# Optimization experiments

Measured on AMD Instinct MI355X. Metric: run time of the kernel, lower is better.

## Reference

```python
import jax, jax.numpy as jnp
import numpy as np

L = 4096   # seq len (Lq == Lk, self-attention)
B = 8      # batch
D = 1024   # d_model
H = 16     # num heads
BUCKET = 32
FUTURE = 0


def setup_inputs() -> dict:
    key = jax.random.key(0)
    ks = jax.random.split(key, 9)
    q = jax.random.normal(ks[0], (L, B, D), jnp.float32)
    k = jax.random.normal(ks[1], (L, B, D), jnp.float32)
    v = jax.random.normal(ks[2], (L, B, D), jnp.float32)
    # one random element per bucket of size BUCKET (deterministic stand-in for
    # the module's no_grad sample_index); pin first sample to 0 so no query row
    # is fully masked under the causal mask.
    nb = L // BUCKET
    offs = jax.random.randint(ks[3], (nb,), 0, BUCKET)
    sampled_index = (jnp.arange(nb, dtype=jnp.int64) * BUCKET + offs).at[0].set(0)
    key_length = jax.random.randint(ks[4], (B,), L // 2, L + 1).astype(jnp.int64)
    # nn.MultiheadAttention params
    in_proj_weight = jax.random.normal(ks[5], (3 * D, D), jnp.float32) * 0.02
    in_proj_bias = jax.random.normal(ks[6], (3 * D,), jnp.float32) * 0.02
    out_w = jax.random.normal(ks[7], (D, D), jnp.float32) * 0.02
    out_b = jax.random.normal(ks[8], (D,), jnp.float32) * 0.02
    return {"q": q, "k": k, "v": v, "key_length": key_length,
            "sampled_index": sampled_index, "in_proj_weight": in_proj_weight,
            "in_proj_bias": in_proj_bias, "out_w": out_w, "out_b": out_b}


def reference(q, k, v, key_length, sampled_index, in_proj_weight, in_proj_bias, out_w, out_b):
    S = sampled_index.shape[0]
    dh = D // H
    # bucket-sampled gather of keys/values: [S, B, D]
    ks_ = k[sampled_index]
    vs_ = v[sampled_index]
    # modify_key_length: number of sampled indices inside each sequence's valid span
    mkl = jnp.sum((sampled_index[None, :] < key_length[:, None]).astype(jnp.int32), axis=1)  # [B]
    key_padding = jnp.arange(S)[None, :] >= mkl[:, None]                                      # [B, S] True = pad
    # causal mask on sampled indices: query i may attend to sample s iff i + future >= s
    causal = (jnp.arange(L)[:, None] + FUTURE) < sampled_index[None, :]                       # [Lq, S] True = masked
    mask = causal[None, None, :, :] | key_padding[:, None, None, :]                           # [B, 1, Lq, S]
    # in-projection (torch linear: x @ W.T + b)
    Wq, Wk, Wv = jnp.split(in_proj_weight, 3, axis=0)
    bq, bk, bv = jnp.split(in_proj_bias, 3)
    qp = (q @ Wq.T + bq).reshape(L, B, H, dh)
    kp = (ks_ @ Wk.T + bk).reshape(S, B, H, dh)
    vp = (vs_ @ Wv.T + bv).reshape(S, B, H, dh)
    scale = 1.0 / np.sqrt(dh).astype(np.float32)
    scores = jnp.einsum('qbhd,kbhd->bhqk', qp, kp) * scale
    scores = jnp.where(mask, -jnp.inf, scores)
    attn = jax.nn.softmax(scores, axis=-1)
    ctx = jnp.einsum('bhqk,kbhd->qbhd', attn, vp).reshape(L, B, D)
    return ctx @ out_w.T + out_b
```

## Files before the change

kernel.cpp:

```cpp
#include <hip/hip_runtime.h>
#include <hip/hip_bf16.h>

#define L_SEQ 4096
#define BATCH 8
#define DMODEL 1024
#define NHEAD 16
#define DHEAD 64
#define NSAMP 128

typedef __attribute__((ext_vector_type(8))) short short8;
typedef __attribute__((ext_vector_type(4))) float f32x4;

static __device__ __forceinline__ unsigned short f2bf(float f) {
    union { float f; unsigned int u; } x; x.f = f;
    unsigned int r = (x.u + 0x7fffu + ((x.u >> 16) & 1u)) >> 16;
    return (unsigned short)r;
}

static __device__ __forceinline__ void gld_lds16(const unsigned short* g,
                                                 unsigned short* l) {
    __builtin_amdgcn_global_load_lds(
        (const __attribute__((address_space(1))) void*)g,
        (__attribute__((address_space(3))) void*)l, 16, 0, 0);
}

__global__ void conv_bf16_kernel(const float* __restrict__ src,
                                 unsigned short* __restrict__ dst, int n4) {
    int idx = blockIdx.x * blockDim.x + threadIdx.x;
    if (idx < n4) {
        float4 v = ((const float4*)src)[idx];
        uint2 pk;
        pk.x = (unsigned)f2bf(v.x) | ((unsigned)f2bf(v.y) << 16);
        pk.y = (unsigned)f2bf(v.z) | ((unsigned)f2bf(v.w) << 16);
        ((uint2*)dst)[idx] = pk;
    }
}

__global__ void gather_bf16_kernel(const float* __restrict__ src,
                                   const int* __restrict__ smp,
                                   unsigned short* __restrict__ dst, int total8) {
    int idx = blockIdx.x * blockDim.x + threadIdx.x;
    if (idx < total8) {
        int s = idx >> 10;
        int rem = idx & 1023;
        const float* g = src + (size_t)smp[s] * (BATCH * DMODEL) + rem * 8;
        float4 v0 = *(const float4*)g;
        float4 v1 = *(const float4*)(g + 4);
        uint4 pk;
        pk.x = (unsigned)f2bf(v0.x) | ((unsigned)f2bf(v0.y) << 16);
        pk.y = (unsigned)f2bf(v0.z) | ((unsigned)f2bf(v0.w) << 16);
        pk.z = (unsigned)f2bf(v1.x) | ((unsigned)f2bf(v1.y) << 16);
        pk.w = (unsigned)f2bf(v1.z) | ((unsigned)f2bf(v1.w) << 16);
        *(uint4*)&dst[(size_t)idx * 8] = pk;
    }
}

__global__ void mkl_kernel(const int* __restrict__ smp,
                           const int* __restrict__ klen, int* __restrict__ mkl) {
    int b = threadIdx.x;
    if (b < BATCH) {
        int kl = klen[b];
        int c = 0;
        for (int s = 0; s < NSAMP; ++s) c += (smp[s] < kl) ? 1 : 0;
        mkl[b] = c;
    }
}

template <bool OUT_F32>
static __device__ __forceinline__ void gemm_body(
    const unsigned short* __restrict__ A, const unsigned short* __restrict__ Bw,
    const float* __restrict__ bias, void* __restrict__ Cp,
    int m0, int n0, int N, int K,
    unsigned short* lA, unsigned short* lB) {
    const int t = threadIdx.x;
    const int wave = t >> 6;
    const int lane = t & 63;
    const int l16 = lane & 15;
    const int quad = lane >> 4;
    const int wm = (wave >> 1) * 64;
    const int wn = (wave & 1) * 64;

    f32x4 acc[4][4];
    #pragma unroll
    for (int i = 0; i < 4; ++i)
        #pragma unroll
        for (int j = 0; j < 4; ++j)
            acc[i][j] = f32x4{0.f, 0.f, 0.f, 0.f};

    const int lin0 = t * 8;
    const int wbase = (t & ~63) * 8;

    for (int k0 = 0; k0 < K; k0 += 64) {
        #pragma unroll
        for (int p = 0; p < 4; ++p) {
            int lin = p * 2048 + lin0;
            int row = lin >> 6, col = lin & 63;
            gld_lds16(A + (size_t)(m0 + row) * K + k0 + col, lA + p * 2048 + wbase);
        }
        #pragma unroll
        for (int p = 0; p < 4; ++p) {
            int lin = p * 2048 + lin0;
            int row = lin >> 6, col = lin & 63;
            gld_lds16(Bw + (size_t)(n0 + row) * K + k0 + col, lB + p * 2048 + wbase);
        }
        __syncthreads();

        #pragma unroll
        for (int kk = 0; kk < 64; kk += 32) {
            short8 af[4], bfr[4];
            #pragma unroll
            for (int mt = 0; mt < 4; ++mt)
                af[mt] = *(const short8*)&lA[(wm + mt * 16 + l16) * 64 + kk + quad * 8];
            #pragma unroll
            for (int nt = 0; nt < 4; ++nt)
                bfr[nt] = *(const short8*)&lB[(wn + nt * 16 + l16) * 64 + kk + quad * 8];
            #pragma unroll
            for (int mt = 0; mt < 4; ++mt)
                #pragma unroll
                for (int nt = 0; nt < 4; ++nt)
                    acc[mt][nt] = __builtin_amdgcn_mfma_f32_16x16x32_bf16(
                        af[mt], bfr[nt], acc[mt][nt], 0, 0, 0);
        }
        __syncthreads();
    }

    #pragma unroll
    for (int mt = 0; mt < 4; ++mt) {
        #pragma unroll
        for (int nt = 0; nt < 4; ++nt) {
            int col = n0 + wn + nt * 16 + l16;
            float bv = bias[col];
            #pragma unroll
            for (int r = 0; r < 4; ++r) {
                int row = m0 + wm + mt * 16 + quad * 4 + r;
                float val = acc[mt][nt][r] + bv;
                if (OUT_F32)
                    ((float*)Cp)[(size_t)row * N + col] = val;
                else
                    ((unsigned short*)Cp)[(size_t)row * N + col] = f2bf(val);
            }
        }
    }
}

__global__ __launch_bounds__(256) void gemm_kv(
    const unsigned short* __restrict__ Ak, const unsigned short* __restrict__ Av,
    const unsigned short* __restrict__ Bk, const unsigned short* __restrict__ Bv,
    const float* __restrict__ bk, const float* __restrict__ bv,
    unsigned short* __restrict__ Ck, unsigned short* __restrict__ Cv) {
    __shared__ __align__(16) unsigned short lA[128 * 64];
    __shared__ __align__(16) unsigned short lB[128 * 64];
    if (blockIdx.z == 0)
        gemm_body<false>(Ak, Bk, bk, Ck, blockIdx.x * 128, blockIdx.y * 128,
                         DMODEL, DMODEL, lA, lB);
    else
        gemm_body<false>(Av, Bv, bv, Cv, blockIdx.x * 128, blockIdx.y * 128,
                         DMODEL, DMODEL, lA, lB);
}

#define GNT 32

template <bool OUT_F32>
__global__ __launch_bounds__(512, 2) void gemm256_kernel(
    const unsigned short* __restrict__ A, const unsigned short* __restrict__ Bw,
    const float* __restrict__ bias, void* __restrict__ Cp)
{
    __shared__ __align__(16) unsigned short ls[4][2][8192];

    const int bid = blockIdx.x;
    const int swz = (bid & 7) * 64 + (bid >> 3);
    const int m0 = (swz >> 2) * 256;
    const int n0 = (swz & 3) * 256;

    const int t = threadIdx.x;
    const int wave = t >> 6, lane = t & 63;
    const int l16 = lane & 15, quad = lane >> 4;
    const int wm = wave >> 2, wn = wave & 3;
    const int wb = wave * 512;

    const int srow = t >> 2;
    const int scol = (t & 3) * 8;
    const unsigned short* a0 = A + (size_t)(m0 + srow) * DMODEL + scol;
    const unsigned short* a1 = a0 + (size_t)128 * DMODEL;
    const unsigned short* b0 = Bw + (size_t)(n0 + srow) * DMODEL + scol;
    const unsigned short* b1 = b0 + (size_t)128 * DMODEL;

    #define STAGE(tk, s) do {                                   \
        gld_lds16(a0 + (tk) * 32, &ls[s][0][wb]);               \
        gld_lds16(a1 + (tk) * 32, &ls[s][0][4096 + wb]);        \
        gld_lds16(b0 + (tk) * 32, &ls[s][1][wb]);               \
        gld_lds16(b1 + (tk) * 32, &ls[s][1][4096 + wb]);        \
    } while (0)

    STAGE(0, 0); STAGE(1, 1); STAGE(2, 2);

    f32x4 acc[8][4];
    #pragma unroll
    for (int i = 0; i < 8; ++i)
        #pragma unroll
        for (int j = 0; j < 4; ++j)
            acc[i][j] = f32x4{0.f, 0.f, 0.f, 0.f};

    const int aoff = (wm * 128 + l16) * 32 + quad * 8;
    const int boff = (wn * 64 + l16) * 32 + quad * 8;

    #pragma unroll
    for (int tk = 0; tk < GNT; ++tk) {
        if (tk < GNT - 2)
            asm volatile("s_waitcnt vmcnt(8)" ::: "memory");
        else if (tk == GNT - 2)
            asm volatile("s_waitcnt vmcnt(4)" ::: "memory");
        else
            asm volatile("s_waitcnt vmcnt(0)" ::: "memory");
        __builtin_amdgcn_s_barrier();

        if (tk + 3 < GNT) STAGE(tk + 3, (tk + 3) & 3);

        const unsigned short* As = &ls[tk & 3][0][0];
        const unsigned short* Bs = &ls[tk & 3][1][0];
        short8 af[8], bq[4];
        #pragma unroll
        for (int nt = 0; nt < 4; ++nt)
            bq[nt] = *(const short8*)&Bs[boff + nt * 512];
        #pragma unroll
        for (int mt = 0; mt < 8; ++mt)
            af[mt] = *(const short8*)&As[aoff + mt * 512];

        __builtin_amdgcn_s_setprio(1);
        #pragma unroll
        for (int mt = 0; mt < 8; ++mt)
            #pragma unroll
            for (int nt = 0; nt < 4; ++nt)
                acc[mt][nt] = __builtin_amdgcn_mfma_f32_16x16x32_bf16(
                    af[mt], bq[nt], acc[mt][nt], 0, 0, 0);
        __builtin_amdgcn_s_setprio(0);
    }
    #undef STAGE

    #pragma unroll
    for (int mt = 0; mt < 8; ++mt) {
        #pragma unroll
        for (int nt = 0; nt < 4; ++nt) {
            int col = n0 + wn * 64 + nt * 16 + l16;
            float bv = bias[col];
            #pragma unroll
            for (int r = 0; r < 4; ++r) {
                int row = m0 + wm * 128 + mt * 16 + quad * 4 + r;
                float val = acc[mt][nt][r] + bv;
                if (OUT_F32)
                    ((float*)Cp)[(size_t)row * DMODEL + col] = val;
                else
                    ((unsigned short*)Cp)[(size_t)row * DMODEL + col] = f2bf(val);
            }
        }
    }
}

#define KST 72
#define VST 136
__global__ __launch_bounds__(256) void attn_kernel(
    const unsigned short* __restrict__ qp,
    const unsigned short* __restrict__ kp,
    const unsigned short* __restrict__ vp,
    const int* __restrict__ smp_g,
    const int* __restrict__ mkl_g,
    unsigned short* __restrict__ ctx)
{
    __shared__ __align__(16) unsigned short kbuf[NSAMP * KST];
    __shared__ __align__(16) unsigned short vT[64 * VST];
    __shared__ __align__(16) unsigned short pbuf[4][16 * VST];
    __shared__ int smp_s[NSAMP];

    const int t = threadIdx.x;
    const int b = blockIdx.y >> 4, h = blockIdx.y & 15;
    const int wave = t >> 6, lane = t & 63;
    const int l16 = lane & 15, quad = lane >> 4;
    const int Lbase = blockIdx.x * 256;
    const int mkl_b = mkl_g[b];

    #pragma unroll
    for (int p = 0; p < 4; ++p) {
        int c = p * 256 + t;
        int s = c >> 3, d0 = (c & 7) * 8;
        *(uint4*)&kbuf[s * KST + d0] =
            *(const uint4*)&kp[((size_t)(s * BATCH + b)) * DMODEL + h * 64 + d0];
    }
    #pragma unroll
    for (int p = 0; p < 4; ++p) {
        int c = p * 256 + t;
        int s = c >> 3, d0 = (c & 7) * 8;
        uint4 pk = *(const uint4*)&vp[((size_t)(s * BATCH + b)) * DMODEL + h * 64 + d0];
        const unsigned short* e = (const unsigned short*)&pk;
        #pragma unroll
        for (int j = 0; j < 8; ++j) vT[(d0 + j) * VST + s] = e[j];
    }
    if (t < NSAMP) smp_s[t] = smp_g[t];
    __syncthreads();

    short8 kf[8][2];
    #pragma unroll
    for (int nt = 0; nt < 8; ++nt) {
        kf[nt][0] = *(const short8*)&kbuf[(nt * 16 + l16) * KST + quad * 8];
        kf[nt][1] = *(const short8*)&kbuf[(nt * 16 + l16) * KST + 32 + quad * 8];
    }

    const float scale = 0.125f;

    for (int qt = 0; qt < 4; ++qt) {
        const int l0 = Lbase + wave * 64 + qt * 16;

        short8 aq0, aq1;
        {
            const unsigned short* qrow =
                qp + ((size_t)(l0 + l16) * BATCH + b) * DMODEL + h * 64;
            aq0 = *(const short8*)&qrow[quad * 8];
            aq1 = *(const short8*)&qrow[32 + quad * 8];
        }

        f32x4 sc[8];
        #pragma unroll
        for (int nt = 0; nt < 8; ++nt) sc[nt] = f32x4{0.f, 0.f, 0.f, 0.f};
        #pragma unroll
        for (int nt = 0; nt < 8; ++nt) {
            sc[nt] = __builtin_amdgcn_mfma_f32_16x16x32_bf16(aq0, kf[nt][0], sc[nt], 0, 0, 0);
            sc[nt] = __builtin_amdgcn_mfma_f32_16x16x32_bf16(aq1, kf[nt][1], sc[nt], 0, 0, 0);
        }

        #pragma unroll
        for (int nt = 0; nt < 8; ++nt) {
            int s = nt * 16 + l16;
            bool pad = (s >= mkl_b);
            int si = smp_s[s];
            #pragma unroll
            for (int r = 0; r < 4; ++r) {
                int lrow = l0 + quad * 4 + r;
                float v = sc[nt][r] * scale;
                if (pad || si > lrow) v = -INFINITY;
                sc[nt][r] = v;
            }
        }
        #pragma unroll
        for (int r = 0; r < 4; ++r) {
            float mx = sc[0][r];
            #pragma unroll
            for (int nt = 1; nt < 8; ++nt) mx = fmaxf(mx, sc[nt][r]);
            #pragma unroll
            for (int off = 1; off < 16; off <<= 1) mx = fmaxf(mx, __shfl_xor(mx, off));
            float sm = 0.f;
            #pragma unroll
            for (int nt = 0; nt < 8; ++nt) {
                float e = __expf(sc[nt][r] - mx);
                sc[nt][r] = e;
                sm += e;
            }
            #pragma unroll
            for (int off = 1; off < 16; off <<= 1) sm += __shfl_xor(sm, off);
            float inv = 1.0f / sm;
            #pragma unroll
            for (int nt = 0; nt < 8; ++nt) sc[nt][r] *= inv;
        }

        #pragma unroll
        for (int nt = 0; nt < 8; ++nt)
            #pragma unroll
            for (int r = 0; r < 4; ++r)
                pbuf[wave][(quad * 4 + r) * VST + nt * 16 + l16] = f2bf(sc[nt][r]);

        f32x4 oc[4];
        #pragma unroll
        for (int dt = 0; dt < 4; ++dt) oc[dt] = f32x4{0.f, 0.f, 0.f, 0.f};
        #pragma unroll
        for (int s0 = 0; s0 < 128; s0 += 32) {
            short8 ap = *(const short8*)&pbuf[wave][l16 * VST + s0 + quad * 8];
            #pragma unroll
            for (int dt = 0; dt < 4; ++dt) {
                short8 bv = *(const short8*)&vT[(dt * 16 + l16) * VST + s0 + quad * 8];
                oc[dt] = __builtin_amdgcn_mfma_f32_16x16x32_bf16(ap, bv, oc[dt], 0, 0, 0);
            }
        }

        #pragma unroll
        for (int dt = 0; dt < 4; ++dt)
            #pragma unroll
            for (int r = 0; r < 4; ++r) {
                int lrow = l0 + quad * 4 + r;
                ctx[((size_t)lrow * BATCH + b) * DMODEL + h * 64 + dt * 16 + l16] =
                    f2bf(oc[dt][r]);
            }
    }
}

extern "C" void kernel_launch(void* const* d_in, const int* in_sizes, int n_in,
                              void* d_out, int out_size, void* d_ws, size_t ws_size,
                              hipStream_t stream) {
    const float* q    = (const float*)d_in[0];
    const float* k    = (const float*)d_in[1];
    const float* v    = (const float*)d_in[2];
    const int*   klen = (const int*)d_in[3];
    const int*   smp  = (const int*)d_in[4];
    const float* ipw  = (const float*)d_in[5];
    const float* ipb  = (const float*)d_in[6];
    const float* ow   = (const float*)d_in[7];
    const float* ob   = (const float*)d_in[8];
    float* out = (float*)d_out;

    char* ws = (char*)d_ws;
    size_t off = 0;
    auto alloc = [&](size_t bytes) -> void* {
        void* p = ws + off;
        off += (bytes + 255) & ~(size_t)255;
        return p;
    };
    unsigned short* w_bf  = (unsigned short*)alloc((size_t)3 * 1024 * 1024 * 2);
    unsigned short* ow_bf = (unsigned short*)alloc((size_t)1024 * 1024 * 2);
    unsigned short* ks_bf = (unsigned short*)alloc((size_t)NSAMP * BATCH * DMODEL * 2);
    unsigned short* vs_bf = (unsigned short*)alloc((size_t)NSAMP * BATCH * DMODEL * 2);
    unsigned short* q_bf  = (unsigned short*)alloc((size_t)L_SEQ * BATCH * DMODEL * 2);
    unsigned short* qp    = (unsigned short*)alloc((size_t)L_SEQ * BATCH * DMODEL * 2);
    unsigned short* kpp   = (unsigned short*)alloc((size_t)NSAMP * BATCH * DMODEL * 2);
    unsigned short* vpp   = (unsigned short*)alloc((size_t)NSAMP * BATCH * DMODEL * 2);
    int*            mkl   = (int*)alloc(256);
    unsigned short* ctx = q_bf;

    conv_bf16_kernel<<<32768, 256, 0, stream>>>(q, q_bf, L_SEQ * BATCH * DMODEL / 4);
    conv_bf16_kernel<<<3072, 256, 0, stream>>>(ipw, w_bf, 3 * 1024 * 1024 / 4);
    conv_bf16_kernel<<<1024, 256, 0, stream>>>(ow, ow_bf, 1024 * 1024 / 4);
    gather_bf16_kernel<<<512, 256, 0, stream>>>(k, smp, ks_bf, NSAMP * BATCH * DMODEL / 8);
    gather_bf16_kernel<<<512, 256, 0, stream>>>(v, smp, vs_bf, NSAMP * BATCH * DMODEL / 8);
    mkl_kernel<<<1, 64, 0, stream>>>(smp, klen, mkl);

    gemm256_kernel<false><<<dim3(512), 512, 0, stream>>>(q_bf, w_bf, ipb, qp);
    gemm_kv<<<dim3(8, 8, 2), 256, 0, stream>>>(
        ks_bf, vs_bf, w_bf + (size_t)1024 * 1024, w_bf + (size_t)2 * 1024 * 1024,
        ipb + 1024, ipb + 2048, kpp, vpp);

    attn_kernel<<<dim3(L_SEQ / 256, BATCH * NHEAD), 256, 0, stream>>>(
        qp, kpp, vpp, smp, mkl, ctx);

    gemm256_kernel<true><<<dim3(512), 512, 0, stream>>>(ctx, ow_bf, ob, out);
}
```

Measured before the change: 601.9 us.

## Restructure 256x256 GEMM mainloop into ping-pong K=64 tiles with swizzled LDS

Rewrites the main loop of the 256x256 bf16 GEMM kernel. K tiles grow from 32 to 64 and the four-stage LDS ring becomes a two-buffer ping-pong. Each K tile is split into four quarter-phases that interleave LDS fragment reads, async global-to-LDS loads for the next tile, and MFMA blocks, with fine-grained waitcnt and barriers between them. An XOR swizzle on the K chunk avoids LDS bank conflicts. The aim is better overlap of memory traffic with MFMA work, at the cost of many more barriers and more complex wait-count bookkeeping.

```diff
diff --git a/kernel.cpp b/kernel.cpp
--- a/kernel.cpp
+++ b/kernel.cpp
@@ -158,14 +158,14 @@
                          DMODEL, DMODEL, lA, lB);
 }
 
-#define GNT 32
+#define GNT 16
 
 template <bool OUT_F32>
 __global__ __launch_bounds__(512, 2) void gemm256_kernel(
     const unsigned short* __restrict__ A, const unsigned short* __restrict__ Bw,
     const float* __restrict__ bias, void* __restrict__ Cp)
 {
-    __shared__ __align__(16) unsigned short ls[4][2][8192];
+    __shared__ __align__(16) unsigned short ls[2][2][256 * 64];
 
     const int bid = blockIdx.x;
     const int swz = (bid & 7) * 64 + (bid >> 3);
@@ -173,26 +173,40 @@
     const int n0 = (swz & 3) * 256;
 
     const int t = threadIdx.x;
-    const int wave = t >> 6, lane = t & 63;
+    const int w = t >> 6, lane = t & 63;
     const int l16 = lane & 15, quad = lane >> 4;
-    const int wm = wave >> 2, wn = wave & 3;
-    const int wb = wave * 512;
-
-    const int srow = t >> 2;
-    const int scol = (t & 3) * 8;
-    const unsigned short* a0 = A + (size_t)(m0 + srow) * DMODEL + scol;
-    const unsigned short* a1 = a0 + (size_t)128 * DMODEL;
-    const unsigned short* b0 = Bw + (size_t)(n0 + srow) * DMODEL + scol;
-    const unsigned short* b1 = b0 + (size_t)128 * DMODEL;
-
-    #define STAGE(tk, s) do {                                   \
-        gld_lds16(a0 + (tk) * 32, &ls[s][0][wb]);               \
-        gld_lds16(a1 + (tk) * 32, &ls[s][0][4096 + wb]);        \
-        gld_lds16(b0 + (tk) * 32, &ls[s][1][wb]);               \
-        gld_lds16(b1 + (tk) * 32, &ls[s][1][4096 + wb]);        \
-    } while (0)
-
-    STAGE(0, 0); STAGE(1, 1); STAGE(2, 2);
+    const int wm = w >> 2, wn = w & 3;
+    const int s8 = l16 & 7;
+    const int lr = lane >> 3;
+    const int kswz = ((lane & 7) ^ lr) * 8;
+
+    const int rA0 = w * 8 + lr;
+    const int rA1 = 128 + w * 8 + lr;
+    const int rA2 = 64 + w * 8 + lr;
+    const int rA3 = 192 + w * 8 + lr;
+    const int blo = w * 8 + (w >= 4 ? 32 : 0);
+    const int rB0 = blo + lr;
+    const int rB1 = blo + 128 + lr;
+    const int rB2 = blo + 32 + lr;
+    const int rB3 = blo + 160 + lr;
+
+    const unsigned short* pA0 = A + (size_t)(m0 + rA0) * DMODEL + kswz;
+    const unsigned short* pA1 = A + (size_t)(m0 + rA1) * DMODEL + kswz;
+    const unsigned short* pA2 = A + (size_t)(m0 + rA2) * DMODEL + kswz;
+    const unsigned short* pA3 = A + (size_t)(m0 + rA3) * DMODEL + kswz;
+    const unsigned short* pB0 = Bw + (size_t)(n0 + rB0) * DMODEL + kswz;
+    const unsigned short* pB1 = Bw + (size_t)(n0 + rB1) * DMODEL + kswz;
+    const unsigned short* pB2 = Bw + (size_t)(n0 + rB2) * DMODEL + kswz;
+    const unsigned short* pB3 = Bw + (size_t)(n0 + rB3) * DMODEL + kswz;
+
+    const int dA0 = (rA0 - lr) * 64;
+    const int dA1 = (rA1 - lr) * 64;
+    const int dA2 = (rA2 - lr) * 64;
+    const int dA3 = (rA3 - lr) * 64;
+    const int dB0 = (rB0 - lr) * 64;
+    const int dB1 = (rB1 - lr) * 64;
+    const int dB2 = (rB2 - lr) * 64;
+    const int dB3 = (rB3 - lr) * 64;
 
     f32x4 acc[8][4];
     #pragma unroll
@@ -201,41 +215,101 @@
         for (int j = 0; j < 4; ++j)
             acc[i][j] = f32x4{0.f, 0.f, 0.f, 0.f};
 
-    const int aoff = (wm * 128 + l16) * 32 + quad * 8;
-    const int boff = (wn * 64 + l16) * 32 + quad * 8;
-
-    #pragma unroll
-    for (int tk = 0; tk < GNT; ++tk) {
-        if (tk < GNT - 2)
-            asm volatile("s_waitcnt vmcnt(8)" ::: "memory");
-        else if (tk == GNT - 2)
-            asm volatile("s_waitcnt vmcnt(4)" ::: "memory");
-        else
-            asm volatile("s_waitcnt vmcnt(0)" ::: "memory");
-        __builtin_amdgcn_s_barrier();
-
-        if (tk + 3 < GNT) STAGE(tk + 3, (tk + 3) & 3);
-
-        const unsigned short* As = &ls[tk & 3][0][0];
-        const unsigned short* Bs = &ls[tk & 3][1][0];
-        short8 af[8], bq[4];
-        #pragma unroll
-        for (int nt = 0; nt < 4; ++nt)
-            bq[nt] = *(const short8*)&Bs[boff + nt * 512];
-        #pragma unroll
-        for (int mt = 0; mt < 8; ++mt)
-            af[mt] = *(const short8*)&As[aoff + mt * 512];
-
-        __builtin_amdgcn_s_setprio(1);
-        #pragma unroll
-        for (int mt = 0; mt < 8; ++mt)
-            #pragma unroll
-            for (int nt = 0; nt < 4; ++nt)
-                acc[mt][nt] = __builtin_amdgcn_mfma_f32_16x16x32_bf16(
-                    af[mt], bq[nt], acc[mt][nt], 0, 0, 0);
-        __builtin_amdgcn_s_setprio(0);
-    }
-    #undef STAGE
+    short8 aq[8];
+    short8 bq[2][4];
+
+    auto rd_a = [&](const unsigned short* As, int mbase) {
+        #pragma unroll
+        for (int mt = 0; mt < 4; ++mt)
+            #pragma unroll
+            for (int kk = 0; kk < 2; ++kk)
+                aq[mt * 2 + kk] = *(const short8*)&As[
+                    (wm * 128 + (mbase + mt) * 16 + l16) * 64 +
+                    ((kk * 4 + quad) ^ s8) * 8];
+    };
+    auto rd_b = [&](int nh, const unsigned short* Bs) {
+        #pragma unroll
+        for (int nt = 0; nt < 2; ++nt)
+            #pragma unroll
+            for (int kk = 0; kk < 2; ++kk)
+                bq[nh][nt * 2 + kk] = *(const short8*)&Bs[
+                    (wn * 64 + (nh * 2 + nt) * 16 + l16) * 64 +
+                    ((kk * 4 + quad) ^ s8) * 8];
+    };
+    auto mm = [&](int mh, int nh) {
+        #pragma unroll
+        for (int kk = 0; kk < 2; ++kk)
+            #pragma unroll
+            for (int mt = 0; mt < 4; ++mt)
+                #pragma unroll
+                for (int nt = 0; nt < 2; ++nt)
+                    acc[mh * 4 + mt][nh * 2 + nt] =
+                        __builtin_amdgcn_mfma_f32_16x16x32_bf16(
+                            aq[mt * 2 + kk], bq[nh][nt * 2 + kk],
+                            acc[mh * 4 + mt][nh * 2 + nt], 0, 0, 0);
+    };
+
+    gld_lds16(pA0, &ls[0][0][dA0]); gld_lds16(pA1, &ls[0][0][dA1]);
+    gld_lds16(pB0, &ls[0][1][dB0]); gld_lds16(pB1, &ls[0][1][dB1]);
+    gld_lds16(pB2, &ls[0][1][dB2]); gld_lds16(pB3, &ls[0][1][dB3]);
+    gld_lds16(pA2, &ls[0][0][dA2]); gld_lds16(pA3, &ls[0][0][dA3]);
+    pA0 += 64; pA1 += 64; pA2 += 64; pA3 += 64;
+    pB0 += 64; pB1 += 64; pB2 += 64; pB3 += 64;
+    asm volatile("s_waitcnt vmcnt(4)" ::: "memory");
+    __builtin_amdgcn_s_barrier();
+
+#define TILE_BODY(CUR, DO_STAGE, VM_A, VM_B, VM_C)                             \
+  {                                                                            \
+    const unsigned short* As = &ls[CUR][0][0];                                 \
+    const unsigned short* Bs = &ls[CUR][1][0];                                 \
+    const int nx = (CUR) ^ 1;                                                  \
+                              \
+    rd_a(As, 0);                                                               \
+    rd_b(0, Bs);                                                               \
+    if (DO_STAGE) { gld_lds16(pA0, &ls[nx][0][dA0]);                           \
+                    gld_lds16(pA1, &ls[nx][0][dA1]); }                         \
+    asm volatile("s_waitcnt lgkmcnt(8)" ::: "memory");                         \
+    __builtin_amdgcn_s_barrier();                                              \
+    asm volatile("s_waitcnt lgkmcnt(0)" ::: "memory");                         \
+    __builtin_amdgcn_s_setprio(1); mm(0, 0); __builtin_amdgcn_s_setprio(0);    \
+    asm volatile("s_waitcnt vmcnt(" VM_A ")" ::: "memory");                    \
+    __builtin_amdgcn_s_barrier();                                              \
+                                     \
+    rd_b(1, Bs);                                                               \
+    if (DO_STAGE) { gld_lds16(pB0, &ls[nx][1][dB0]);                           \
+                    gld_lds16(pB1, &ls[nx][1][dB1]); }                         \
+    __builtin_amdgcn_s_barrier();                                              \
+    asm volatile("s_waitcnt lgkmcnt(0)" ::: "memory");                         \
+    __builtin_amdgcn_s_setprio(1); mm(0, 1); __builtin_amdgcn_s_setprio(0);    \
+    asm volatile("s_waitcnt vmcnt(" VM_B ")" ::: "memory");                    \
+    __builtin_amdgcn_s_barrier();                                              \
+                                     \
+    rd_a(As, 4);                                                               \
+    if (DO_STAGE) { gld_lds16(pB2, &ls[nx][1][dB2]);                           \
+                    gld_lds16(pB3, &ls[nx][1][dB3]); }                         \
+    __builtin_amdgcn_s_barrier();                                              \
+    asm volatile("s_waitcnt lgkmcnt(0)" ::: "memory");                         \
+    __builtin_amdgcn_s_setprio(1); mm(1, 0); __builtin_amdgcn_s_setprio(0);    \
+    __builtin_amdgcn_s_barrier();                                              \
+                             \
+    if (DO_STAGE) { gld_lds16(pA2, &ls[nx][0][dA2]);                           \
+                    gld_lds16(pA3, &ls[nx][0][dA3]); }                         \
+    __builtin_amdgcn_s_barrier();                                              \
+    __builtin_amdgcn_s_setprio(1); mm(1, 1); __builtin_amdgcn_s_setprio(0);    \
+    if (VM_C) { asm volatile("s_waitcnt vmcnt(4)" ::: "memory"); }             \
+    __builtin_amdgcn_s_barrier();                                              \
+  }
+
+    int cur = 0;
+    #pragma unroll 1
+    for (int tt = 0; tt < GNT - 1; ++tt) {
+        TILE_BODY(cur, true, "4", "4", true);
+        pA0 += 64; pA1 += 64; pA2 += 64; pA3 += 64;
+        pB0 += 64; pB1 += 64; pB2 += 64; pB3 += 64;
+        cur ^= 1;
+    }
+    TILE_BODY(cur, false, "2", "0", false);
+#undef TILE_BODY
 
     #pragma unroll
     for (int mt = 0; mt < 8; ++mt) {
```

New measurement: 584.7 us. 1.03x faster.
